# Performance work log

Measured on AMD Instinct MI355X. Metric: run time of the kernel, lower is better.

## Reference

```python
import jax, jax.numpy as jnp
import numpy as np

M = 100000   # BS*L nodes
D_IN = 256   # in_d
D_OUT = 256  # out_d
E = 1024     # number of edges; indices index the out_d axis (faithful to source quirk)


def setup_inputs() -> dict:
    key = jax.random.key(0)
    k1, k2, k3 = jax.random.split(key, 3)
    node_features = jax.random.normal(k1, (1, M, D_IN), dtype=jnp.float32)
    W = jax.random.normal(k2, (D_OUT, D_IN), dtype=jnp.float32) * (1.0 / np.sqrt(D_IN))
    b = jnp.zeros((D_OUT,), dtype=jnp.float32)
    edge_mapping = jax.random.randint(k3, (2, E), 0, D_OUT, dtype=jnp.int64)
    batch_lens = jnp.ones((M, 1), dtype=jnp.float32)
    return {"node_features": node_features, "W": W, "b": b,
            "edge_mapping": edge_mapping, "batch_lens": batch_lens}


def reference(node_features, W, b, edge_mapping, batch_lens):
    # fc: [1, M, in_d] -> [1, M, out_d]
    h = jnp.einsum('bmi,oi->bmo', node_features, W) + b
    residual = h                              # [1, M, D_OUT]
    hf = jnp.swapaxes(h, 1, 2)[0]             # [D_OUT, M]  (transpose(2,1).squeeze(0))
    gathered = hf[edge_mapping[1]]            # [E, M]      (index_select dim=0)
    agg = jnp.zeros_like(hf).at[edge_mapping[0]].add(gathered)  # scatter-add, [D_OUT, M]
    new_nf = agg.T                            # [M, D_OUT]
    out = (new_nf + residual) / batch_lens    # broadcast -> [1, M, D_OUT]
    return out
```

## Files before the change

### kernel.cpp

```cpp
#include <hip/hip_runtime.h>
#include <cstdint>

constexpr int D = 256;
constexpr int TM = 128;

typedef __bf16 bf16x8 __attribute__((ext_vector_type(8)));
typedef float  f32x4  __attribute__((ext_vector_type(4)));

__global__ void prep_copy(const float* __restrict__ W, const float* __restrict__ b,
                          float* __restrict__ W2, float* __restrict__ b2) {
    int i = blockIdx.x * 256 + threadIdx.x;
    W2[i] = W[i];
    if (blockIdx.x == 0) b2[threadIdx.x] = b[threadIdx.x];
}

__global__ void prep_edges(const int* __restrict__ em, int E,
                           const float* __restrict__ W, const float* __restrict__ b,
                           float* __restrict__ W2, float* __restrict__ b2) {
    int e = blockIdx.x;
    int k = threadIdx.x;
    int dst = em[e];
    int src = em[E + e];
    atomicAdd(&W2[dst * D + k], W[src * D + k]);
    if (k == 0) atomicAdd(&b2[dst], b[src]);
}

__global__ void prep_convert(const float* __restrict__ W2, ushort* __restrict__ Wh,
                             ushort* __restrict__ Wl) {
    int i = blockIdx.x * 256 + threadIdx.x;
    int o = i >> 8, k = i & 255;
    float x = W2[i];
    uint32_t u  = __float_as_uint(x);
    uint32_t hu = u & 0xFFFF0000u;
    float r = x - __uint_as_float(hu);
    uint32_t ru = __float_as_uint(r);
    uint32_t lu = ru + 0x7FFFu + ((ru >> 16) & 1u);
    int kc = k >> 5, kk = k & 31, q = kk >> 3, j = kk & 7;
    int o16b = o >> 4;
    int lane = (o & 15) + 16 * q;
    int idx = kc * 8192 + (o16b * 64 + lane) * 8 + j;
    Wh[idx] = (ushort)(hu >> 16);
    Wl[idx] = (ushort)(lu >> 16);
}

__device__ __forceinline__ void gl_lds16(const ushort* g, ushort* l) {
    __builtin_amdgcn_global_load_lds(
        (const __attribute__((address_space(1))) uint32_t*)g,
        (__attribute__((address_space(3))) uint32_t*)l, 16, 0, 0);
}

__device__ __forceinline__ void cvt8(const float4& f0, const float4& f1,
                                     uint4& hi, uint4& lo) {
    float xs[8] = {f0.x, f0.y, f0.z, f0.w, f1.x, f1.y, f1.z, f1.w};
    uint32_t h[8], l[8];
    #pragma unroll
    for (int j = 0; j < 8; ++j) {
        uint32_t u  = __float_as_uint(xs[j]);
        uint32_t hu = u & 0xFFFF0000u;
        h[j] = hu;
        float r = xs[j] - __uint_as_float(hu);
        uint32_t ru = __float_as_uint(r);
        l[j] = ru + 0x7FFFu + ((ru >> 16) & 1u);
    }
    hi = make_uint4((h[0] >> 16) | (h[1] & 0xFFFF0000u),
                    (h[2] >> 16) | (h[3] & 0xFFFF0000u),
                    (h[4] >> 16) | (h[5] & 0xFFFF0000u),
                    (h[6] >> 16) | (h[7] & 0xFFFF0000u));
    lo = make_uint4((l[0] >> 16) | (l[1] & 0xFFFF0000u),
                    (l[2] >> 16) | (l[3] & 0xFFFF0000u),
                    (l[4] >> 16) | (l[5] & 0xFFFF0000u),
                    (l[6] >> 16) | (l[7] & 0xFFFF0000u));
}

__global__ __launch_bounds__(256, 2) void resgcn_mfma(
    const float* __restrict__ X, const ushort* __restrict__ Whg,
    const ushort* __restrict__ Wlg, const float* __restrict__ b2,
    const float* __restrict__ blen, float* __restrict__ out, int M)
{
    __shared__ ushort Xh[8][64][8];
    __shared__ ushort Xl[8][64][8];
    __shared__ ushort Wh[16][64][8];
    __shared__ ushort Wl[16][64][8];

    const int tid  = threadIdx.x;
    const int lane = tid & 63;
    const int wv   = tid >> 6;
    const int m0   = blockIdx.x * TM;

    const int sm = tid >> 1;
    const int sh = tid & 1;
    int srow = m0 + sm; if (srow >= M) srow = M - 1;
    const float* xrow = X + (size_t)srow * D + sh * 16;
    const int m16b = sm >> 4;
    const int mlow = sm & 15;

    f32x4 acc[8][4];
    #pragma unroll
    for (int a = 0; a < 8; ++a)
        #pragma unroll
        for (int b = 0; b < 4; ++b) acc[a][b] = (f32x4){0.f, 0.f, 0.f, 0.f};

    for (int kc = 0; kc < 8; ++kc) {
        __syncthreads();

        {
            const ushort* gh = Whg + kc * 8192;
            const ushort* gl = Wlg + kc * 8192;
            ushort* lh = &Wh[0][0][0];
            ushort* ll = &Wl[0][0][0];
            #pragma unroll
            for (int i = 0; i < 4; ++i) {
                int off = (i * 256 + tid) * 8;
                gl_lds16(gh + off, lh + off);
                gl_lds16(gl + off, ll + off);
            }
        }

        {
            const float* p = xrow + kc * 32;
            float4 f0 = *(const float4*)(p + 0);
            float4 f1 = *(const float4*)(p + 4);
            float4 f2 = *(const float4*)(p + 8);
            float4 f3 = *(const float4*)(p + 12);
            uint4 h0, l0, h1, l1;
            cvt8(f0, f1, h0, l0);
            cvt8(f2, f3, h1, l1);
            const int q0 = sh * 2, q1 = sh * 2 + 1;
            *(uint4*)&Xh[m16b][mlow + 16 * q0][0] = h0;
            *(uint4*)&Xl[m16b][mlow + 16 * q0][0] = l0;
            *(uint4*)&Xh[m16b][mlow + 16 * q1][0] = h1;
            *(uint4*)&Xl[m16b][mlow + 16 * q1][0] = l1;
        }

        __syncthreads();

        bf16x8 bh[4], blo[4];
        #pragma unroll
        for (int b = 0; b < 4; ++b) {
            bh[b]  = *(const bf16x8*)&Wh[wv * 4 + b][lane][0];
            blo[b] = *(const bf16x8*)&Wl[wv * 4 + b][lane][0];
        }
        #pragma unroll
        for (int a = 0; a < 8; ++a) {
            bf16x8 ah = *(const bf16x8*)&Xh[a][lane][0];
            bf16x8 al = *(const bf16x8*)&Xl[a][lane][0];
            #pragma unroll
            for (int b = 0; b < 4; ++b) {
                acc[a][b] = __builtin_amdgcn_mfma_f32_16x16x32_bf16(ah, bh[b],  acc[a][b], 0, 0, 0);
                acc[a][b] = __builtin_amdgcn_mfma_f32_16x16x32_bf16(al, bh[b],  acc[a][b], 0, 0, 0);
                acc[a][b] = __builtin_amdgcn_mfma_f32_16x16x32_bf16(ah, blo[b], acc[a][b], 0, 0, 0);
            }
        }
    }

    const int col = lane & 15;
    const int rq  = lane >> 4;
    float bias[4];
    #pragma unroll
    for (int b = 0; b < 4; ++b) bias[b] = b2[(wv * 4 + b) * 16 + col];

    #pragma unroll
    for (int a = 0; a < 8; ++a) {
        #pragma unroll
        for (int r = 0; r < 4; ++r) {
            int m = m0 + a * 16 + rq * 4 + r;
            if (m < M) {
                float inv = 1.0f / blen[m];
                #pragma unroll
                for (int b = 0; b < 4; ++b) {
                    int o = (wv * 4 + b) * 16 + col;
                    out[(size_t)m * D + o] = (acc[a][b][r] + bias[b]) * inv;
                }
            }
        }
    }
}

extern "C" void kernel_launch(void* const* d_in, const int* in_sizes, int n_in,
                              void* d_out, int out_size, void* d_ws, size_t ws_size,
                              hipStream_t stream) {
    (void)n_in; (void)out_size; (void)ws_size;
    const float* X  = (const float*)d_in[0];
    const float* W  = (const float*)d_in[1];
    const float* b  = (const float*)d_in[2];
    const int*   em = (const int*)d_in[3];
    const float* bl = (const float*)d_in[4];
    float* out = (float*)d_out;

    const int M = in_sizes[0] / D;
    const int E = in_sizes[3] / 2;

    float*  W2 = (float*)d_ws;
    float*  b2 = W2 + D * D;
    ushort* Wh = (ushort*)(b2 + D);
    ushort* Wl = Wh + D * D;

    prep_copy<<<D * D / 256, 256, 0, stream>>>(W, b, W2, b2);
    prep_edges<<<E, D, 0, stream>>>(em, E, W, b, W2, b2);
    prep_convert<<<D * D / 256, 256, 0, stream>>>(W2, Wh, Wl);

    int mblocks = (M + TM - 1) / TM;
    resgcn_mfma<<<mblocks, 256, 0, stream>>>(X, Wh, Wl, b2, bl, out, M);
}
```

Baseline: 218.9 us.

## Drop LDS staging; load X and W fragments directly from global into registers

Removes the shared-memory staging of X and W and both block barriers per K-chunk. Each wave now loads its W fragments straight from the pre-swizzled global layout and loads and converts its own X rows per MFMA tile, with the K loop unrolled by two. This avoids LDS traffic and synchronisation, but each of the four waves now loads and converts the same X data, which quadruples X global reads (mostly served from cache) and the split-conversion ALU work.

```diff
diff --git a/kernel.cpp b/kernel.cpp
--- a/kernel.cpp
+++ b/kernel.cpp
@@ -43,14 +43,8 @@
     Wl[idx] = (ushort)(lu >> 16);
 }
 
-__device__ __forceinline__ void gl_lds16(const ushort* g, ushort* l) {
-    __builtin_amdgcn_global_load_lds(
-        (const __attribute__((address_space(1))) uint32_t*)g,
-        (__attribute__((address_space(3))) uint32_t*)l, 16, 0, 0);
-}
-
-__device__ __forceinline__ void cvt8(const float4& f0, const float4& f1,
-                                     uint4& hi, uint4& lo) {
+__device__ __forceinline__ void cvt8v(const float4& f0, const float4& f1,
+                                      bf16x8& hi, bf16x8& lo) {
     float xs[8] = {f0.x, f0.y, f0.z, f0.w, f1.x, f1.y, f1.z, f1.w};
     uint32_t h[8], l[8];
     #pragma unroll
@@ -62,14 +56,17 @@
         uint32_t ru = __float_as_uint(r);
         l[j] = ru + 0x7FFFu + ((ru >> 16) & 1u);
     }
-    hi = make_uint4((h[0] >> 16) | (h[1] & 0xFFFF0000u),
-                    (h[2] >> 16) | (h[3] & 0xFFFF0000u),
-                    (h[4] >> 16) | (h[5] & 0xFFFF0000u),
-                    (h[6] >> 16) | (h[7] & 0xFFFF0000u));
-    lo = make_uint4((l[0] >> 16) | (l[1] & 0xFFFF0000u),
-                    (l[2] >> 16) | (l[3] & 0xFFFF0000u),
-                    (l[4] >> 16) | (l[5] & 0xFFFF0000u),
-                    (l[6] >> 16) | (l[7] & 0xFFFF0000u));
+    union { uint4 u; bf16x8 v; } ch, cl;
+    ch.u = make_uint4((h[0] >> 16) | (h[1] & 0xFFFF0000u),
+                      (h[2] >> 16) | (h[3] & 0xFFFF0000u),
+                      (h[4] >> 16) | (h[5] & 0xFFFF0000u),
+                      (h[6] >> 16) | (h[7] & 0xFFFF0000u));
+    cl.u = make_uint4((l[0] >> 16) | (l[1] & 0xFFFF0000u),
+                      (l[2] >> 16) | (l[3] & 0xFFFF0000u),
+                      (l[4] >> 16) | (l[5] & 0xFFFF0000u),
+                      (l[6] >> 16) | (l[7] & 0xFFFF0000u));
+    hi = ch.v;
+    lo = cl.v;
 }
 
 __global__ __launch_bounds__(256, 2) void resgcn_mfma(
@@ -77,22 +74,24 @@
     const ushort* __restrict__ Wlg, const float* __restrict__ b2,
     const float* __restrict__ blen, float* __restrict__ out, int M)
 {
-    __shared__ ushort Xh[8][64][8];
-    __shared__ ushort Xl[8][64][8];
-    __shared__ ushort Wh[16][64][8];
-    __shared__ ushort Wl[16][64][8];
-
     const int tid  = threadIdx.x;
     const int lane = tid & 63;
     const int wv   = tid >> 6;
     const int m0   = blockIdx.x * TM;
 
-    const int sm = tid >> 1;
-    const int sh = tid & 1;
-    int srow = m0 + sm; if (srow >= M) srow = M - 1;
-    const float* xrow = X + (size_t)srow * D + sh * 16;
-    const int m16b = sm >> 4;
-    const int mlow = sm & 15;
+    const int rlow = lane & 15;
+    const int kq   = lane >> 4;
+
+    const float* xbase[8];
+    #pragma unroll
+    for (int a = 0; a < 8; ++a) {
+        int r = m0 + a * 16 + rlow;
+        if (r >= M) r = M - 1;
+        xbase[a] = X + (size_t)r * D + kq * 8;
+    }
+
+    const ushort* whb = Whg + ((wv * 4) * 64 + lane) * 8;
+    const ushort* wlb = Wlg + ((wv * 4) * 64 + lane) * 8;
 
     f32x4 acc[8][4];
     #pragma unroll
@@ -100,55 +99,26 @@
         #pragma unroll
         for (int b = 0; b < 4; ++b) acc[a][b] = (f32x4){0.f, 0.f, 0.f, 0.f};
 
+    #pragma unroll 2
     for (int kc = 0; kc < 8; ++kc) {
-        __syncthreads();
-
-        {
-            const ushort* gh = Whg + kc * 8192;
-            const ushort* gl = Wlg + kc * 8192;
-            ushort* lh = &Wh[0][0][0];
-            ushort* ll = &Wl[0][0][0];
-            #pragma unroll
-            for (int i = 0; i < 4; ++i) {
-                int off = (i * 256 + tid) * 8;
-                gl_lds16(gh + off, lh + off);
-                gl_lds16(gl + off, ll + off);
-            }
-        }
-
-        {
-            const float* p = xrow + kc * 32;
-            float4 f0 = *(const float4*)(p + 0);
-            float4 f1 = *(const float4*)(p + 4);
-            float4 f2 = *(const float4*)(p + 8);
-            float4 f3 = *(const float4*)(p + 12);
-            uint4 h0, l0, h1, l1;
-            cvt8(f0, f1, h0, l0);
-            cvt8(f2, f3, h1, l1);
-            const int q0 = sh * 2, q1 = sh * 2 + 1;
-            *(uint4*)&Xh[m16b][mlow + 16 * q0][0] = h0;
-            *(uint4*)&Xl[m16b][mlow + 16 * q0][0] = l0;
-            *(uint4*)&Xh[m16b][mlow + 16 * q1][0] = h1;
-            *(uint4*)&Xl[m16b][mlow + 16 * q1][0] = l1;
-        }
-
-        __syncthreads();
-
-        bf16x8 bh[4], blo[4];
+        bf16x8 bh[4], bl[4];
         #pragma unroll
         for (int b = 0; b < 4; ++b) {
-            bh[b]  = *(const bf16x8*)&Wh[wv * 4 + b][lane][0];
-            blo[b] = *(const bf16x8*)&Wl[wv * 4 + b][lane][0];
+            bh[b] = *(const bf16x8*)(whb + kc * 8192 + b * 512);
+            bl[b] = *(const bf16x8*)(wlb + kc * 8192 + b * 512);
         }
         #pragma unroll
         for (int a = 0; a < 8; ++a) {
-            bf16x8 ah = *(const bf16x8*)&Xh[a][lane][0];
-            bf16x8 al = *(const bf16x8*)&Xl[a][lane][0];
+            const float* p = xbase[a] + kc * 32;
+            float4 f0 = *(const float4*)(p + 0);
+            float4 f1 = *(const float4*)(p + 4);
+            bf16x8 ah, al;
+            cvt8v(f0, f1, ah, al);
             #pragma unroll
             for (int b = 0; b < 4; ++b) {
-                acc[a][b] = __builtin_amdgcn_mfma_f32_16x16x32_bf16(ah, bh[b],  acc[a][b], 0, 0, 0);
-                acc[a][b] = __builtin_amdgcn_mfma_f32_16x16x32_bf16(al, bh[b],  acc[a][b], 0, 0, 0);
-                acc[a][b] = __builtin_amdgcn_mfma_f32_16x16x32_bf16(ah, blo[b], acc[a][b], 0, 0, 0);
+                acc[a][b] = __builtin_amdgcn_mfma_f32_16x16x32_bf16(ah, bh[b], acc[a][b], 0, 0, 0);
+                acc[a][b] = __builtin_amdgcn_mfma_f32_16x16x32_bf16(al, bh[b], acc[a][b], 0, 0, 0);
+                acc[a][b] = __builtin_amdgcn_mfma_f32_16x16x32_bf16(ah, bl[b], acc[a][b], 0, 0, 0);
             }
         }
     }
```

Result: slower. 280.0 us (+27.9%).
